# Kernel tuning notes

Measured on AMD Instinct MI355X. Metric: run time of the kernel, lower is better.

The kernel has to match this reference:

```python
import jax, jax.numpy as jnp
import numpy as np

N = 50000
E = 800000
D = 128
EPS = 1e-5


def setup_inputs() -> dict:
    key = jax.random.key(0)
    ks = jax.random.split(key, 12)
    x = jax.random.normal(ks[0], (N, D), dtype=jnp.float32)
    pos = jax.random.normal(ks[1], (N, 3), dtype=jnp.float32)
    edge_index = jax.random.randint(ks[2], (2, E), 0, N, dtype=jnp.int32)
    s_e1 = 1.0 / np.sqrt(2 * D + 1)
    s_d = 1.0 / np.sqrt(D)
    s_n1 = 1.0 / np.sqrt(2 * D)
    return {
        "x": x,
        "pos": pos,
        "edge_index": edge_index,
        "W1e": jax.random.uniform(ks[3], (2 * D + 1, D), jnp.float32, -s_e1, s_e1),
        "b1e": jnp.zeros((D,), jnp.float32),
        "W2e": jax.random.uniform(ks[4], (D, D), jnp.float32, -s_d, s_d),
        "b2e": jnp.zeros((D,), jnp.float32),
        "W1n": jax.random.uniform(ks[5], (2 * D, D), jnp.float32, -s_n1, s_n1),
        "b1n": jnp.zeros((D,), jnp.float32),
        "W2n": jax.random.uniform(ks[6], (D, D), jnp.float32, -s_d, s_d),
        "b2n": jnp.zeros((D,), jnp.float32),
        "gamma": jnp.ones((D,), jnp.float32),
        "beta": jnp.zeros((D,), jnp.float32),
    }


def reference(x, pos, edge_index, W1e, b1e, W2e, b2e, W1n, b1n, W2n, b2n, gamma, beta):
    row, col = edge_index[0], edge_index[1]
    # gather + relative position
    rel_pos = pos[row] - pos[col]                       # [E, 3]
    dist2 = jnp.sum(rel_pos * rel_pos, axis=1, keepdims=True)  # [E, 1]
    edge_input = jnp.concatenate([x[row], x[col], dist2], axis=1)  # [E, 2D+1]
    # 2-layer edge MLP with SiLU activations
    h = jax.nn.silu(edge_input @ W1e + b1e)
    edge_feat = jax.nn.silu(h @ W2e + b2e)              # [E, D]
    # scatter-add aggregation onto source nodes (row)
    agg = jax.ops.segment_sum(edge_feat, row, num_segments=x.shape[0])  # [N, D]
    # 2-layer node MLP (SiLU only after first layer)
    node_in = jnp.concatenate([x, agg], axis=1)         # [N, 2D]
    update = jax.nn.silu(node_in @ W1n + b1n) @ W2n + b2n
    # dropout omitted (inference/eval mode)
    # LayerNorm(x + update)
    y = x + update
    mu = jnp.mean(y, axis=-1, keepdims=True)
    var = jnp.var(y, axis=-1, keepdims=True)
    return (y - mu) * jax.lax.rsqrt(var + EPS) * gamma + beta
```

## Files before the change

kernel.cpp:

```cpp
#include <hip/hip_runtime.h>
#include <hip/hip_bf16.h>
#include <math.h>

#define D 128
#define NND 50000
#define NE 800000
#define NB1 196
#define TPITCH 152

typedef __attribute__((ext_vector_type(8))) short shortx8;
typedef __attribute__((ext_vector_type(4))) float floatx4;

__device__ __forceinline__ float silu_f(float v) {
    return v * __builtin_amdgcn_rcpf(1.0f + __expf(-v));
}
__device__ __forceinline__ unsigned short f2bf(float f) {
    union { float f; unsigned int u; } v; v.f = f;
    unsigned int u = v.u;
    u += 0x7fffu + ((u >> 16) & 1u);
    return (unsigned short)(u >> 16);
}
__device__ __forceinline__ void unpk(unsigned int u, float& lo, float& hi) {
    union { unsigned int x; float f; } a, b;
    a.x = u << 16;
    b.x = u & 0xffff0000u;
    lo = a.f; hi = b.f;
}

__global__ void zero_kernel(float4* __restrict__ p, int n4) {
    int i = blockIdx.x * blockDim.x + threadIdx.x;
    float4 z = make_float4(0.f, 0.f, 0.f, 0.f);
    for (; i < n4; i += gridDim.x * blockDim.x) p[i] = z;
}

__global__ void hist_kernel(const int* __restrict__ ei, int* __restrict__ deg) {
    int e = blockIdx.x * 256 + threadIdx.x;
    atomicAdd(&deg[ei[e]], 1);
}

__global__ void scan1_kernel(const int* __restrict__ deg,
                             int* __restrict__ part, int* __restrict__ bsum) {
    __shared__ int s[256];
    const int tid = threadIdx.x;
    const int i = blockIdx.x * 256 + tid;
    int v = (i < NND) ? deg[i] : 0;
    s[tid] = v;
    __syncthreads();
    #pragma unroll
    for (int off = 1; off < 256; off <<= 1) {
        int t = (tid >= off) ? s[tid - off] : 0;
        __syncthreads();
        s[tid] += t;
        __syncthreads();
    }
    part[i] = s[tid] - v;
    if (tid == 255) bsum[blockIdx.x] = s[255];
}

__global__ void scan2_kernel(const int* __restrict__ bsum, int* __restrict__ boff) {
    __shared__ int s[256];
    const int tid = threadIdx.x;
    int v = (tid < NB1) ? bsum[tid] : 0;
    s[tid] = v;
    __syncthreads();
    #pragma unroll
    for (int off = 1; off < 256; off <<= 1) {
        int t = (tid >= off) ? s[tid - off] : 0;
        __syncthreads();
        s[tid] += t;
        __syncthreads();
    }
    if (tid < NB1) boff[tid] = s[tid] - v;
}

__global__ void scan3_kernel(const int* __restrict__ part, const int* __restrict__ boff,
                             int* __restrict__ rowptr, int* __restrict__ cursor) {
    int i = blockIdx.x * 256 + threadIdx.x;
    if (i < NND) {
        int v = part[i] + boff[i >> 8];
        rowptr[i] = v;
        cursor[i] = v;
    } else if (i == NND) {
        rowptr[NND] = NE;
    }
}

__global__ void scatter_kernel(const int* __restrict__ ei, const float* __restrict__ pos,
                               int* __restrict__ cursor,
                               int* __restrict__ ecol, int* __restrict__ erow,
                               float* __restrict__ ed2) {
    int e = blockIdx.x * 256 + threadIdx.x;
    int r = ei[e], c = ei[NE + e];
    float dx = pos[r * 3 + 0] - pos[c * 3 + 0];
    float dy = pos[r * 3 + 1] - pos[c * 3 + 1];
    float dz = pos[r * 3 + 2] - pos[c * 3 + 2];
    int slot = atomicAdd(&cursor[r], 1);
    ecol[slot] = c;
    erow[slot] = r;
    ed2[slot] = dx * dx + dy * dy + dz * dz;
}

__global__ void wswz_kernel(const float* __restrict__ W,
                            unsigned short* __restrict__ Wf) {
    int f = blockIdx.x * 256 + threadIdx.x;
    int j    = f & 7;
    int mrow = (f >> 3) & 15;
    int n    = (f >> 7) & 7;
    int rest = f >> 10;
    int quad = rest & 3;
    int ks   = rest >> 2;
    int col = n * 16 + mrow;
    int k   = ks * 32 + quad * 8 + j;
    Wf[f] = f2bf(W[k * D + col]);
}

__global__ void wlf_kernel(const float* __restrict__ W1e,
                           unsigned short* __restrict__ wlf) {
    int t = threadIdx.x;
    wlf[t] = f2bf(W1e[256 * D + t]);
}

__global__ void x2bf_kernel(const float4* __restrict__ x4, uint2* __restrict__ xbf) {
    int i = blockIdx.x * 256 + threadIdx.x;
    float4 v = x4[i];
    uint2 o;
    o.x = (unsigned int)f2bf(v.x) | ((unsigned int)f2bf(v.y) << 16);
    o.y = (unsigned int)f2bf(v.z) | ((unsigned int)f2bf(v.w) << 16);
    xbf[i] = o;
}

__global__ __launch_bounds__(256) void precompute_kernel(
        const unsigned short* __restrict__ xbf,
        const unsigned short* __restrict__ w1f,
        const float* __restrict__ b1e,
        unsigned short* __restrict__ A,
        unsigned short* __restrict__ Bm) {
    const int t    = threadIdx.x;
    const int wv   = t >> 6;
    const int lane = t & 63;
    const int mrow = lane & 15;
    const int quad = lane >> 4;
    const int tile = blockIdx.x * 4 + wv;
    if (tile >= 3125) return;
    const int n0 = tile * 16;

    const uint4* xrow = (const uint4*)(xbf + ((size_t)(n0 + mrow) << 7));
    const uint4* wp   = (const uint4*)w1f;

    floatx4 accA[8], accB[8];
    #pragma unroll
    for (int n = 0; n < 8; ++n) {
        accA[n] = (floatx4){0.f, 0.f, 0.f, 0.f};
        accB[n] = (floatx4){0.f, 0.f, 0.f, 0.f};
    }

    #pragma unroll
    for (int s = 0; s < 4; ++s) {
        union { uint4 u; shortx8 v; } af;
        af.u = xrow[s * 4 + quad];
        const int baseA = (s * 4 + quad) * 128 + mrow;
        const int baseB = ((s + 4) * 4 + quad) * 128 + mrow;
        #pragma unroll
        for (int n = 0; n < 8; ++n) {
            union { uint4 u; shortx8 v; } bfA, bfB;
            bfA.u = wp[baseA + n * 16];
            bfB.u = wp[baseB + n * 16];
            accA[n] = __builtin_amdgcn_mfma_f32_16x16x32_bf16(af.v, bfA.v, accA[n], 0, 0, 0);
            accB[n] = __builtin_amdgcn_mfma_f32_16x16x32_bf16(af.v, bfB.v, accB[n], 0, 0, 0);
        }
    }

    float bb[8];
    #pragma unroll
    for (int n = 0; n < 8; ++n) bb[n] = b1e[n * 16 + mrow];

    #pragma unroll
    for (int reg = 0; reg < 4; ++reg) {
        const int node = n0 + quad * 4 + reg;
        #pragma unroll
        for (int n = 0; n < 8; ++n) {
            const int col = n * 16 + mrow;
            A[(size_t)node * D + col]  = f2bf(accA[n][reg] + bb[n]);
            Bm[(size_t)node * D + col] = f2bf(accB[n][reg]);
        }
    }
}

__global__ __launch_bounds__(256, 2) void edgemlp_kernel(
        const unsigned short* __restrict__ Abf,
        const unsigned short* __restrict__ Bbf,
        const int* __restrict__ erow,
        const int* __restrict__ ecol,
        const float* __restrict__ ed2,
        const unsigned short* __restrict__ wlf,
        const unsigned short* __restrict__ W2f,
        const float* __restrict__ b2e,
        unsigned short* __restrict__ ef) {
    const int t    = threadIdx.x;
    const int wv   = t >> 6;
    const int lane = t & 63;
    const int mrow = lane & 15;
    const int quad = lane >> 4;
    const int tile = blockIdx.x * 4 + wv;
    const int e0   = tile * 16;
    const int eme  = e0 + mrow;

    const int   r  = erow[eme];
    const int   c  = ecol[eme];
    const float d2 = ed2[eme];

    const uint4* arow = (const uint4*)(Abf + ((size_t)r << 7));
    const uint4* brow = (const uint4*)(Bbf + ((size_t)c << 7));
    const uint4* wlq  = (const uint4*)wlf;
    const uint4* w2p  = (const uint4*)W2f;

    floatx4 acc[8];
    #pragma unroll
    for (int k = 0; k < 8; ++k) acc[k] = (floatx4){0.f, 0.f, 0.f, 0.f};

    #pragma unroll
    for (int s = 0; s < 4; ++s) {
        uint4 au = arow[s * 4 + quad];
        uint4 bu = brow[s * 4 + quad];
        uint4 wu = wlq[s * 4 + quad];

        float a0, a1, a2, a3, a4, a5, a6, a7;
        float q0, q1, q2, q3, q4, q5, q6, q7;
        float w0, w1, w2, w3, w4, w5, w6, w7;
        unpk(au.x, a0, a1); unpk(au.y, a2, a3);
        unpk(au.z, a4, a5); unpk(au.w, a6, a7);
        unpk(bu.x, q0, q1); unpk(bu.y, q2, q3);
        unpk(bu.z, q4, q5); unpk(bu.w, q6, q7);
        unpk(wu.x, w0, w1); unpk(wu.y, w2, w3);
        unpk(wu.z, w4, w5); unpk(wu.w, w6, w7);

        float h0 = silu_f(fmaf(d2, w0, a0 + q0));
        float h1 = silu_f(fmaf(d2, w1, a1 + q1));
        float h2 = silu_f(fmaf(d2, w2, a2 + q2));
        float h3 = silu_f(fmaf(d2, w3, a3 + q3));
        float h4 = silu_f(fmaf(d2, w4, a4 + q4));
        float h5 = silu_f(fmaf(d2, w5, a5 + q5));
        float h6 = silu_f(fmaf(d2, w6, a6 + q6));
        float h7 = silu_f(fmaf(d2, w7, a7 + q7));

        union { shortx8 v; __hip_bfloat162 p[4]; } af;
        af.p[0] = __float22bfloat162_rn(float2{h0, h1});
        af.p[1] = __float22bfloat162_rn(float2{h2, h3});
        af.p[2] = __float22bfloat162_rn(float2{h4, h5});
        af.p[3] = __float22bfloat162_rn(float2{h6, h7});

        const int base = (s * 4 + quad) * 128 + mrow;
        #pragma unroll
        for (int k = 0; k < 8; ++k) {
            union { uint4 u; shortx8 v; } bf;
            bf.u = w2p[base + k * 16];
            acc[k] = __builtin_amdgcn_mfma_f32_16x16x32_bf16(af.v, bf.v, acc[k], 0, 0, 0);
        }
    }

    float bias[8];
    #pragma unroll
    for (int k = 0; k < 8; ++k) bias[k] = b2e[k * 16 + mrow];

    #pragma unroll
    for (int reg = 0; reg < 4; ++reg) {
        const int edge = e0 + quad * 4 + reg;
        union { uint4 u; __hip_bfloat162 p[4]; } ov;
        #pragma unroll
        for (int n = 0; n < 4; ++n) {
            float v0 = silu_f(acc[2 * n + 0][reg] + bias[2 * n + 0]);
            float v1 = silu_f(acc[2 * n + 1][reg] + bias[2 * n + 1]);
            ov.p[n] = __float22bfloat162_rn(float2{v0, v1});
        }
        *(uint4*)(ef + (((size_t)edge) << 7) + mrow * 8) = ov.u;
    }
}

__global__ __launch_bounds__(256) void aggsum_kernel(
        const unsigned short* __restrict__ ef,
        const int* __restrict__ rowptr,
        unsigned short* __restrict__ aggbf) {
    const int t    = threadIdx.x;
    const int lane = t & 63;
    const int node = blockIdx.x * 4 + (t >> 6);
    const int start = rowptr[node];
    const int end   = rowptr[node + 1];
    const unsigned int* efw = (const unsigned int*)ef;

    float s0a = 0.f, s1a = 0.f, s0b = 0.f, s1b = 0.f;
    float s0c = 0.f, s1c = 0.f, s0d = 0.f, s1d = 0.f;
    int e = start;
    for (; e + 4 <= end; e += 4) {
        unsigned int ua = efw[(size_t)(e + 0) * 64 + lane];
        unsigned int ub = efw[(size_t)(e + 1) * 64 + lane];
        unsigned int uc = efw[(size_t)(e + 2) * 64 + lane];
        unsigned int ud = efw[(size_t)(e + 3) * 64 + lane];
        float a0, a1, b0, b1, c0, c1, d0, d1;
        unpk(ua, a0, a1); unpk(ub, b0, b1);
        unpk(uc, c0, c1); unpk(ud, d0, d1);
        s0a += a0; s1a += a1; s0b += b0; s1b += b1;
        s0c += c0; s1c += c1; s0d += d0; s1d += d1;
    }
    for (; e < end; ++e) {
        unsigned int ua = efw[(size_t)e * 64 + lane];
        float a0, a1;
        unpk(ua, a0, a1);
        s0a += a0; s1a += a1;
    }
    const float s0 = (s0a + s0b) + (s0c + s0d);
    const float s1 = (s1a + s1b) + (s1c + s1d);

    const int p0 = lane * 2, p1 = lane * 2 + 1;
    const int k0 = (p0 & 7) * 16 + (p0 >> 3);
    const int k1 = (p1 & 7) * 16 + (p1 >> 3);
    aggbf[((size_t)node << 7) + k0] = f2bf(s0);
    aggbf[((size_t)node << 7) + k1] = f2bf(s1);
}

__global__ __launch_bounds__(256, 2) void edgeagg_kernel(
        const unsigned short* __restrict__ Abf,
        const unsigned short* __restrict__ Bbf,
        const int* __restrict__ rowptr,
        const int* __restrict__ ecol,
        const float* __restrict__ ed2,
        const unsigned short* __restrict__ wlf,
        const unsigned short* __restrict__ W2f,
        const float* __restrict__ b2e,
        unsigned short* __restrict__ aggbf) {
    const int t    = threadIdx.x;
    const int wv   = t >> 6;
    const int lane = t & 63;
    const int mrow = lane & 15;
    const int quad = lane >> 4;
    const int node = blockIdx.x * 4 + wv;

    const int start = rowptr[node];
    const int d     = rowptr[node + 1] - start;

    const uint4* arow = (const uint4*)(Abf + ((size_t)node << 7));
    const uint4* wlq  = (const uint4*)wlf;
    uint4 au[4], wlu[4];
    #pragma unroll
    for (int s = 0; s < 4; ++s) {
        au[s]  = arow[s * 4 + quad];
        wlu[s] = wlq[s * 4 + quad];
    }
    float bias[8];
    #pragma unroll
    for (int k = 0; k < 8; ++k) bias[k] = b2e[k * 16 + mrow];

    float nacc[8];
    #pragma unroll
    for (int k = 0; k < 8; ++k) nacc[k] = 0.f;

    const uint4* w2p = (const uint4*)W2f;

    for (int tb = 0; tb < d; tb += 16) {
        const int  ei16 = tb + mrow;
        const bool ve   = ei16 < d;
        const int  idx  = start + (ve ? ei16 : 0);
        const int  c    = ecol[idx];
        float d2        = ed2[idx];
        d2 = ve ? d2 : 0.f;
        const uint4* brow = (const uint4*)(Bbf + ((size_t)c << 7));

        floatx4 acc[8];
        #pragma unroll
        for (int k = 0; k < 8; ++k) acc[k] = (floatx4){0.f, 0.f, 0.f, 0.f};

        #pragma unroll
        for (int s = 0; s < 4; ++s) {
            uint4 bu = brow[s * 4 + quad];

            float a0, a1, a2, a3, a4, a5, a6, a7;
            float q0, q1, q2, q3, q4, q5, q6, q7;
            float w0, w1, w2, w3, w4, w5, w6, w7;
            unpk(au[s].x, a0, a1); unpk(au[s].y, a2, a3);
            unpk(au[s].z, a4, a5); unpk(au[s].w, a6, a7);
            unpk(bu.x, q0, q1); unpk(bu.y, q2, q3);
            unpk(bu.z, q4, q5); unpk(bu.w, q6, q7);
            unpk(wlu[s].x, w0, w1); unpk(wlu[s].y, w2, w3);
            unpk(wlu[s].z, w4, w5); unpk(wlu[s].w, w6, w7);

            float h0 = silu_f(fmaf(d2, w0, a0 + q0));
            float h1 = silu_f(fmaf(d2, w1, a1 + q1));
            float h2 = silu_f(fmaf(d2, w2, a2 + q2));
            float h3 = silu_f(fmaf(d2, w3, a3 + q3));
            float h4 = silu_f(fmaf(d2, w4, a4 + q4));
            float h5 = silu_f(fmaf(d2, w5, a5 + q5));
            float h6 = silu_f(fmaf(d2, w6, a6 + q6));
            float h7 = silu_f(fmaf(d2, w7, a7 + q7));

            union { shortx8 v; __hip_bfloat162 p[4]; } af;
            af.p[0] = __float22bfloat162_rn(float2{h0, h1});
            af.p[1] = __float22bfloat162_rn(float2{h2, h3});
            af.p[2] = __float22bfloat162_rn(float2{h4, h5});
            af.p[3] = __float22bfloat162_rn(float2{h6, h7});

            const int base = (s * 4 + quad) * 128 + mrow;
            #pragma unroll
            for (int k = 0; k < 8; ++k) {
                union { uint4 u; shortx8 v; } bf;
                bf.u = w2p[base + k * 16];
                acc[k] = __builtin_amdgcn_mfma_f32_16x16x32_bf16(af.v, bf.v, acc[k], 0, 0, 0);
            }
        }

        #pragma unroll
        for (int reg = 0; reg < 4; ++reg) {
            const bool vr = (tb + quad * 4 + reg) < d;
            #pragma unroll
            for (int k = 0; k < 8; ++k)
                nacc[k] += vr ? silu_f(acc[k][reg] + bias[k]) : 0.f;
        }
    }

    #pragma unroll
    for (int k = 0; k < 8; ++k) {
        float v = nacc[k];
        v += __shfl_xor(v, 16);
        v += __shfl_xor(v, 32);
        nacc[k] = v;
    }
    const int n8a = quad * 2, n8b = quad * 2 + 1;
    aggbf[(size_t)node * D + n8a * 16 + mrow] = f2bf(nacc[n8a]);
    aggbf[(size_t)node * D + n8b * 16 + mrow] = f2bf(nacc[n8b]);
}

__global__ __launch_bounds__(64) void node_kernel(
        const unsigned short* __restrict__ xbf,
        const unsigned short* __restrict__ aggbf,
        const unsigned short* __restrict__ w1nf,
        const float* __restrict__ b1n,
        const unsigned short* __restrict__ w2nf,
        const float* __restrict__ b2n,
        const float* __restrict__ x,
        const float* __restrict__ gamma,
        const float* __restrict__ beta,
        float* __restrict__ out) {
    __shared__ __align__(16) unsigned short ts[16 * TPITCH];
    const int lane = threadIdx.x;
    const int mrow = lane & 15;
    const int quad = lane >> 4;
    const int n0 = blockIdx.x * 16;

    const uint4* xrow = (const uint4*)(xbf + ((size_t)(n0 + mrow) << 7));
    const uint4* grow = (const uint4*)(aggbf + ((size_t)(n0 + mrow) << 7));
    const uint4* w1p  = (const uint4*)w1nf;
    const uint4* w2p  = (const uint4*)w2nf;

    floatx4 acc[8];
    #pragma unroll
    for (int n = 0; n < 8; ++n) {
        float b = b1n[n * 16 + mrow];
        acc[n] = (floatx4){b, b, b, b};
    }

    #pragma unroll
    for (int s = 0; s < 4; ++s) {
        union { uint4 u; shortx8 v; } af;
        af.u = xrow[s * 4 + quad];
        const int base = (s * 4 + quad) * 128 + mrow;
        #pragma unroll
        for (int n = 0; n < 8; ++n) {
            union { uint4 u; shortx8 v; } bf;
            bf.u = w1p[base + n * 16];
            acc[n] = __builtin_amdgcn_mfma_f32_16x16x32_bf16(af.v, bf.v, acc[n], 0, 0, 0);
        }
    }
    #pragma unroll
    for (int s = 0; s < 4; ++s) {
        union { uint4 u; shortx8 v; } af;
        af.u = grow[s * 4 + quad];
        const int base = ((s + 4) * 4 + quad) * 128 + mrow;
        #pragma unroll
        for (int n = 0; n < 8; ++n) {
            union { uint4 u; shortx8 v; } bf;
            bf.u = w1p[base + n * 16];
            acc[n] = __builtin_amdgcn_mfma_f32_16x16x32_bf16(af.v, bf.v, acc[n], 0, 0, 0);
        }
    }

    #pragma unroll
    for (int reg = 0; reg < 4; ++reg) {
        const int m = quad * 4 + reg;
        #pragma unroll
        for (int n = 0; n < 8; ++n)
            ts[m * TPITCH + n * 16 + mrow] = f2bf(silu_f(acc[n][reg]));
    }
    __syncthreads();

    floatx4 acc2[8];
    #pragma unroll
    for (int n = 0; n < 8; ++n) {
        float b = b2n[n * 16 + mrow];
        acc2[n] = (floatx4){b, b, b, b};
    }
    #pragma unroll
    for (int s = 0; s < 4; ++s) {
        shortx8 af2 = *(const shortx8*)((const char*)ts +
                        mrow * (TPITCH * 2) + (s * 4 + quad) * 16);
        const int base = (s * 4 + quad) * 128 + mrow;
        #pragma unroll
        for (int n = 0; n < 8; ++n) {
            union { uint4 u; shortx8 v; } bf;
            bf.u = w2p[base + n * 16];
            acc2[n] = __builtin_amdgcn_mfma_f32_16x16x32_bf16(af2, bf.v, acc2[n], 0, 0, 0);
        }
    }

    float g[8], bt[8];
    #pragma unroll
    for (int n = 0; n < 8; ++n) {
        g[n]  = gamma[n * 16 + mrow];
        bt[n] = beta[n * 16 + mrow];
    }
    #pragma unroll
    for (int reg = 0; reg < 4; ++reg) {
        const int node = n0 + quad * 4 + reg;
        float u[8];
        float s1 = 0.f, s2 = 0.f;
        #pragma unroll
        for (int n = 0; n < 8; ++n) {
            u[n] = acc2[n][reg] + x[(size_t)node * D + n * 16 + mrow];
            s1 += u[n];
            s2 += u[n] * u[n];
        }
        #pragma unroll
        for (int off = 1; off < 16; off <<= 1) {
            s1 += __shfl_xor(s1, off);
            s2 += __shfl_xor(s2, off);
        }
        const float mu  = s1 * (1.f / 128.f);
        const float var = s2 * (1.f / 128.f) - mu * mu;
        const float rs  = rsqrtf(var + 1e-5f);
        #pragma unroll
        for (int n = 0; n < 8; ++n)
            out[(size_t)node * D + n * 16 + mrow] = (u[n] - mu) * rs * g[n] + bt[n];
    }
}

extern "C" void kernel_launch(void* const* d_in, const int* in_sizes, int n_in,
                              void* d_out, int out_size, void* d_ws, size_t ws_size,
                              hipStream_t stream) {
    const float* x     = (const float*)d_in[0];
    const float* pos   = (const float*)d_in[1];
    const int*   ei    = (const int*)d_in[2];
    const float* W1e   = (const float*)d_in[3];
    const float* b1e   = (const float*)d_in[4];
    const float* W2e   = (const float*)d_in[5];
    const float* b2e   = (const float*)d_in[6];
    const float* W1n   = (const float*)d_in[7];
    const float* b1n   = (const float*)d_in[8];
    const float* W2n   = (const float*)d_in[9];
    const float* b2n   = (const float*)d_in[10];
    const float* gamma = (const float*)d_in[11];
    const float* beta  = (const float*)d_in[12];
    float* out = (float*)d_out;

    unsigned short* Abf    = (unsigned short*)d_ws;
    unsigned short* Bbf    = Abf + (size_t)NND * D;
    unsigned short* aggbf  = Bbf + (size_t)NND * D;
    unsigned short* xbf    = aggbf + (size_t)NND * D;
    unsigned short* w1f    = xbf + (size_t)NND * D;
    unsigned short* w1nf   = w1f + 256 * D;
    unsigned short* w2f    = w1nf + 256 * D;
    unsigned short* w2nf   = w2f + D * D;
    unsigned short* wlf    = w2nf + D * D;
    int*            deg    = (int*)(wlf + 128);
    int*            part   = deg + 50176;
    int*            bsum   = part + 50176;
    int*            boff   = bsum + 256;
    int*            rowptr = boff + 256;
    int*            cursor = rowptr + 50004;
    int*            ecol   = cursor + 50000;
    int*            erow   = ecol + NE;
    float*          ed2    = (float*)(erow + NE);
    unsigned short* ef     = (unsigned short*)(ed2 + NE);

    const size_t need_big = ((size_t)((unsigned short*)(ed2 + NE) - (unsigned short*)d_ws)) * 2
                            + (size_t)NE * D * 2;
    const bool bigws = ws_size >= need_big;

    zero_kernel<<<64, 256, 0, stream>>>((float4*)deg, 50176 / 4);
    hist_kernel<<<NE / 256, 256, 0, stream>>>(ei, deg);
    scan1_kernel<<<NB1, 256, 0, stream>>>(deg, part, bsum);
    scan2_kernel<<<1, 256, 0, stream>>>(bsum, boff);
    scan3_kernel<<<197, 256, 0, stream>>>(part, boff, rowptr, cursor);
    scatter_kernel<<<NE / 256, 256, 0, stream>>>(ei, pos, cursor, ecol, erow, ed2);

    wswz_kernel<<<(256 * D) / 256, 256, 0, stream>>>(W1e, w1f);
    wswz_kernel<<<(256 * D) / 256, 256, 0, stream>>>(W1n, w1nf);
    wswz_kernel<<<(D * D) / 256, 256, 0, stream>>>(W2e, w2f);
    wswz_kernel<<<(D * D) / 256, 256, 0, stream>>>(W2n, w2nf);
    wlf_kernel<<<1, 128, 0, stream>>>(W1e, wlf);
    x2bf_kernel<<<(NND * D / 4) / 256, 256, 0, stream>>>((const float4*)x, (uint2*)xbf);

    precompute_kernel<<<782, 256, 0, stream>>>(xbf, w1f, b1e, Abf, Bbf);

    if (bigws) {
        edgemlp_kernel<<<NE / 16 / 4, 256, 0, stream>>>(Abf, Bbf, erow, ecol, ed2,
                                                        wlf, w2f, b2e, ef);
        aggsum_kernel<<<NND / 4, 256, 0, stream>>>(ef, rowptr, aggbf);
    } else {
        edgeagg_kernel<<<NND / 4, 256, 0, stream>>>(Abf, Bbf, rowptr, ecol, ed2,
                                                    wlf, w2f, b2e, aggbf);
    }

    node_kernel<<<NND / 16, 64, 0, stream>>>(xbf, aggbf, w1nf, b1n, w2nf, b2n,
                                             x, gamma, beta, out);
}
```

Measured before the change: 395.4 us.

## Fuse weight-swizzle launches, vectorize aggsum loads, store aggregate in fp32

Merges the four weight-swizzle launches and the wlf launch into one kernel. Rewrites aggsum so each lane loads 16-byte uint4 chunks, with four edges processed per wave iteration and combined by cross-lane shuffles. The aggregate is now stored as fp32 and converted to bf16 inside node_kernel. Also drops the occupancy hint on edgemlp, shrinks the zero_kernel grid, and reorders the workspace layout. Fewer launches and wider loads are traded against doubled aggregate traffic and possibly lower edgemlp occupancy.

```diff
diff --git a/kernel.cpp b/kernel.cpp
--- a/kernel.cpp
+++ b/kernel.cpp
@@ -100,9 +100,22 @@
     ed2[slot] = dx * dx + dy * dy + dz * dz;
 }
 
-__global__ void wswz_kernel(const float* __restrict__ W,
-                            unsigned short* __restrict__ Wf) {
-    int f = blockIdx.x * 256 + threadIdx.x;
+__global__ void wswzall_kernel(const float* __restrict__ W1e, const float* __restrict__ W1n,
+                               const float* __restrict__ W2e, const float* __restrict__ W2n,
+                               unsigned short* __restrict__ w1f, unsigned short* __restrict__ w1nf,
+                               unsigned short* __restrict__ w2f, unsigned short* __restrict__ w2nf,
+                               unsigned short* __restrict__ wlf) {
+    const int b = blockIdx.x;
+    const float* W; unsigned short* Wf; int lb;
+    if (b < 128)      { W = W1e; Wf = w1f;  lb = b; }
+    else if (b < 256) { W = W1n; Wf = w1nf; lb = b - 128; }
+    else if (b < 320) { W = W2e; Wf = w2f;  lb = b - 256; }
+    else if (b < 384) { W = W2n; Wf = w2nf; lb = b - 320; }
+    else {
+        if (threadIdx.x < 128) wlf[threadIdx.x] = f2bf(W1e[256 * D + threadIdx.x]);
+        return;
+    }
+    int f = lb * 256 + threadIdx.x;
     int j    = f & 7;
     int mrow = (f >> 3) & 15;
     int n    = (f >> 7) & 7;
@@ -112,12 +125,6 @@
     int col = n * 16 + mrow;
     int k   = ks * 32 + quad * 8 + j;
     Wf[f] = f2bf(W[k * D + col]);
-}
-
-__global__ void wlf_kernel(const float* __restrict__ W1e,
-                           unsigned short* __restrict__ wlf) {
-    int t = threadIdx.x;
-    wlf[t] = f2bf(W1e[256 * D + t]);
 }
 
 __global__ void x2bf_kernel(const float4* __restrict__ x4, uint2* __restrict__ xbf) {
@@ -186,7 +193,7 @@
     }
 }
 
-__global__ __launch_bounds__(256, 2) void edgemlp_kernel(
+__global__ __launch_bounds__(256) void edgemlp_kernel(
         const unsigned short* __restrict__ Abf,
         const unsigned short* __restrict__ Bbf,
         const int* __restrict__ erow,
@@ -279,42 +286,44 @@
 __global__ __launch_bounds__(256) void aggsum_kernel(
         const unsigned short* __restrict__ ef,
         const int* __restrict__ rowptr,
-        unsigned short* __restrict__ aggbf) {
+        float* __restrict__ aggf) {
     const int t    = threadIdx.x;
     const int lane = t & 63;
     const int node = blockIdx.x * 4 + (t >> 6);
     const int start = rowptr[node];
     const int end   = rowptr[node + 1];
-    const unsigned int* efw = (const unsigned int*)ef;
-
-    float s0a = 0.f, s1a = 0.f, s0b = 0.f, s1b = 0.f;
-    float s0c = 0.f, s1c = 0.f, s0d = 0.f, s1d = 0.f;
-    int e = start;
-    for (; e + 4 <= end; e += 4) {
-        unsigned int ua = efw[(size_t)(e + 0) * 64 + lane];
-        unsigned int ub = efw[(size_t)(e + 1) * 64 + lane];
-        unsigned int uc = efw[(size_t)(e + 2) * 64 + lane];
-        unsigned int ud = efw[(size_t)(e + 3) * 64 + lane];
-        float a0, a1, b0, b1, c0, c1, d0, d1;
-        unpk(ua, a0, a1); unpk(ub, b0, b1);
-        unpk(uc, c0, c1); unpk(ud, d0, d1);
-        s0a += a0; s1a += a1; s0b += b0; s1b += b1;
-        s0c += c0; s1c += c1; s0d += d0; s1d += d1;
-    }
-    for (; e < end; ++e) {
-        unsigned int ua = efw[(size_t)e * 64 + lane];
-        float a0, a1;
-        unpk(ua, a0, a1);
-        s0a += a0; s1a += a1;
-    }
-    const float s0 = (s0a + s0b) + (s0c + s0d);
-    const float s1 = (s1a + s1b) + (s1c + s1d);
-
-    const int p0 = lane * 2, p1 = lane * 2 + 1;
-    const int k0 = (p0 & 7) * 16 + (p0 >> 3);
-    const int k1 = (p1 & 7) * 16 + (p1 >> 3);
-    aggbf[((size_t)node << 7) + k0] = f2bf(s0);
-    aggbf[((size_t)node << 7) + k1] = f2bf(s1);
+    const int sub  = lane >> 4;
+    const int j    = lane & 15;
+
+    const uint4* ef4 = (const uint4*)ef;
+
+    float s[8];
+    #pragma unroll
+    for (int i = 0; i < 8; ++i) s[i] = 0.f;
+
+    for (int e = start; e < end; e += 4) {
+        const int  er    = e + sub;
+        const bool valid = er < end;
+        const int  safe  = valid ? er : start;
+        uint4 u = ef4[(size_t)safe * 16 + j];
+        float f0, f1, f2, f3, f4, f5, f6, f7;
+        unpk(u.x, f0, f1); unpk(u.y, f2, f3);
+        unpk(u.z, f4, f5); unpk(u.w, f6, f7);
+        if (valid) {
+            s[0] += f0; s[1] += f1; s[2] += f2; s[3] += f3;
+            s[4] += f4; s[5] += f5; s[6] += f6; s[7] += f7;
+        }
+    }
+    #pragma unroll
+    for (int i = 0; i < 8; ++i) {
+        s[i] += __shfl_xor(s[i], 16);
+        s[i] += __shfl_xor(s[i], 32);
+    }
+    if (sub == 0) {
+        float* dst = aggf + ((size_t)node << 7) + j;
+        #pragma unroll
+        for (int i = 0; i < 8; ++i) dst[i * 16] = s[i];
+    }
 }
 
 __global__ __launch_bounds__(256, 2) void edgeagg_kernel(
@@ -326,7 +335,7 @@
         const unsigned short* __restrict__ wlf,
         const unsigned short* __restrict__ W2f,
         const float* __restrict__ b2e,
-        unsigned short* __restrict__ aggbf) {
+        float* __restrict__ aggf) {
     const int t    = threadIdx.x;
     const int wv   = t >> 6;
     const int lane = t & 63;
@@ -423,13 +432,13 @@
         nacc[k] = v;
     }
     const int n8a = quad * 2, n8b = quad * 2 + 1;
-    aggbf[(size_t)node * D + n8a * 16 + mrow] = f2bf(nacc[n8a]);
-    aggbf[(size_t)node * D + n8b * 16 + mrow] = f2bf(nacc[n8b]);
+    aggf[(size_t)node * D + n8a * 16 + mrow] = nacc[n8a];
+    aggf[(size_t)node * D + n8b * 16 + mrow] = nacc[n8b];
 }
 
 __global__ __launch_bounds__(64) void node_kernel(
         const unsigned short* __restrict__ xbf,
-        const unsigned short* __restrict__ aggbf,
+        const float* __restrict__ aggf,
         const unsigned short* __restrict__ w1nf,
         const float* __restrict__ b1n,
         const unsigned short* __restrict__ w2nf,
@@ -444,10 +453,10 @@
     const int quad = lane >> 4;
     const int n0 = blockIdx.x * 16;
 
-    const uint4* xrow = (const uint4*)(xbf + ((size_t)(n0 + mrow) << 7));
-    const uint4* grow = (const uint4*)(aggbf + ((size_t)(n0 + mrow) << 7));
-    const uint4* w1p  = (const uint4*)w1nf;
-    const uint4* w2p  = (const uint4*)w2nf;
+    const uint4*  xrow  = (const uint4*)(xbf + ((size_t)(n0 + mrow) << 7));
+    const float4* growf = (const float4*)(aggf + ((size_t)(n0 + mrow) << 7));
+    const uint4*  w1p   = (const uint4*)w1nf;
+    const uint4*  w2p   = (const uint4*)w2nf;
 
     floatx4 acc[8];
     #pragma unroll
@@ -470,8 +479,13 @@
     }
     #pragma unroll
     for (int s = 0; s < 4; ++s) {
-        union { uint4 u; shortx8 v; } af;
-        af.u = grow[s * 4 + quad];
+        float4 g0 = growf[(s * 4 + quad) * 2 + 0];
+        float4 g1 = growf[(s * 4 + quad) * 2 + 1];
+        union { shortx8 v; __hip_bfloat162 p[4]; } af;
+        af.p[0] = __float22bfloat162_rn(float2{g0.x, g0.y});
+        af.p[1] = __float22bfloat162_rn(float2{g0.z, g0.w});
+        af.p[2] = __float22bfloat162_rn(float2{g1.x, g1.y});
+        af.p[3] = __float22bfloat162_rn(float2{g1.z, g1.w});
         const int base = ((s + 4) * 4 + quad) * 128 + mrow;
         #pragma unroll
         for (int n = 0; n < 8; ++n) {
@@ -558,16 +572,8 @@
     const float* beta  = (const float*)d_in[12];
     float* out = (float*)d_out;
 
-    unsigned short* Abf    = (unsigned short*)d_ws;
-    unsigned short* Bbf    = Abf + (size_t)NND * D;
-    unsigned short* aggbf  = Bbf + (size_t)NND * D;
-    unsigned short* xbf    = aggbf + (size_t)NND * D;
-    unsigned short* w1f    = xbf + (size_t)NND * D;
-    unsigned short* w1nf   = w1f + 256 * D;
-    unsigned short* w2f    = w1nf + 256 * D;
-    unsigned short* w2nf   = w2f + D * D;
-    unsigned short* wlf    = w2nf + D * D;
-    int*            deg    = (int*)(wlf + 128);
+    float*          aggf   = (float*)d_ws;
+    int*            deg    = (int*)(aggf + (size_t)NND * D);
     int*            part   = deg + 50176;
     int*            bsum   = part + 50176;
     int*            boff   = bsum + 256;
@@ -576,24 +582,29 @@
     int*            ecol   = cursor + 50000;
     int*            erow   = ecol + NE;
     float*          ed2    = (float*)(erow + NE);
-    unsigned short* ef     = (unsigned short*)(ed2 + NE);
-
-    const size_t need_big = ((size_t)((unsigned short*)(ed2 + NE) - (unsigned short*)d_ws)) * 2
-                            + (size_t)NE * D * 2;
+    unsigned short* Abf    = (unsigned short*)(ed2 + NE);
+    unsigned short* Bbf    = Abf + (size_t)NND * D;
+    unsigned short* xbf    = Bbf + (size_t)NND * D;
+    unsigned short* w1f    = xbf + (size_t)NND * D;
+    unsigned short* w1nf   = w1f + 256 * D;
+    unsigned short* w2f    = w1nf + 256 * D;
+    unsigned short* w2nf   = w2f + D * D;
+    unsigned short* wlf    = w2nf + D * D;
+    unsigned short* ef     = wlf + 128;
+
+    const size_t need_big = (size_t)((char*)(ef + (size_t)NE * D) - (char*)d_ws);
     const bool bigws = ws_size >= need_big;
 
-    zero_kernel<<<64, 256, 0, stream>>>((float4*)deg, 50176 / 4);
+    zero_kernel<<<49, 256, 0, stream>>>((float4*)deg, 50176 / 4);
+
     hist_kernel<<<NE / 256, 256, 0, stream>>>(ei, deg);
     scan1_kernel<<<NB1, 256, 0, stream>>>(deg, part, bsum);
     scan2_kernel<<<1, 256, 0, stream>>>(bsum, boff);
     scan3_kernel<<<197, 256, 0, stream>>>(part, boff, rowptr, cursor);
     scatter_kernel<<<NE / 256, 256, 0, stream>>>(ei, pos, cursor, ecol, erow, ed2);
 
-    wswz_kernel<<<(256 * D) / 256, 256, 0, stream>>>(W1e, w1f);
-    wswz_kernel<<<(256 * D) / 256, 256, 0, stream>>>(W1n, w1nf);
-    wswz_kernel<<<(D * D) / 256, 256, 0, stream>>>(W2e, w2f);
-    wswz_kernel<<<(D * D) / 256, 256, 0, stream>>>(W2n, w2nf);
-    wlf_kernel<<<1, 128, 0, stream>>>(W1e, wlf);
+    wswzall_kernel<<<385, 256, 0, stream>>>(W1e, W1n, W2e, W2n,
+                                            w1f, w1nf, w2f, w2nf, wlf);
     x2bf_kernel<<<(NND * D / 4) / 256, 256, 0, stream>>>((const float4*)x, (uint2*)xbf);
 
     precompute_kernel<<<782, 256, 0, stream>>>(xbf, w1f, b1e, Abf, Bbf);
@@ -601,12 +612,12 @@
     if (bigws) {
         edgemlp_kernel<<<NE / 16 / 4, 256, 0, stream>>>(Abf, Bbf, erow, ecol, ed2,
                                                         wlf, w2f, b2e, ef);
-        aggsum_kernel<<<NND / 4, 256, 0, stream>>>(ef, rowptr, aggbf);
+        aggsum_kernel<<<NND / 4, 256, 0, stream>>>(ef, rowptr, aggf);
     } else {
         edgeagg_kernel<<<NND / 4, 256, 0, stream>>>(Abf, Bbf, rowptr, ecol, ed2,
-                                                    wlf, w2f, b2e, aggbf);
-    }
-
-    node_kernel<<<NND / 16, 64, 0, stream>>>(xbf, aggbf, w1nf, b1n, w2nf, b2n,
+                                                    wlf, w2f, b2e, aggf);
+    }
+
+    node_kernel<<<NND / 16, 64, 0, stream>>>(xbf, aggf, w1nf, b1n, w2nf, b2n,
                                              x, gamma, beta, out);
 }
```

Result: slower. 516.3 us (+30.6%).
